# Kernel tuning notes

Hardware: AMD Instinct MI355X
Metric: run time of the kernel (lower is better)

Reference implementation:

```python
import jax, jax.numpy as jnp
import numpy as np

K_NEIGHBORS = 5
EPS = 1e-12  # torch F.normalize eps


def _l2_normalize(x):
    n = jnp.linalg.norm(x, axis=-1, keepdims=True)
    return x / jnp.maximum(n, EPS)


def setup_inputs() -> dict:
    key = jax.random.key(0)
    k1, k2, k3, k4 = jax.random.split(key, 4)
    B, D = 256, 512
    N, A = 50000, 8
    return {
        "z_flowed": jax.random.normal(k1, (B, D), dtype=jnp.float32),
        "target_attrs": jax.random.randint(k2, (B, A), 0, 3, dtype=jnp.int32),
        "train_embeddings": jax.random.normal(k3, (N, D), dtype=jnp.float32),
        "train_attributes": jax.random.randint(k4, (N, A), 0, 3, dtype=jnp.int32),
    }


def reference(z_flowed, target_attrs, train_embeddings, train_attributes):
    B = z_flowed.shape[0]
    A = target_attrs.shape[1]
    z_norm = _l2_normalize(z_flowed)          # [B, D]
    train_norm = _l2_normalize(train_embeddings)  # [N, D]

    # batched attribute match: [B, N] count of matching attributes
    match_score = (train_attributes[None, :, :] == target_attrs[:, None, :]).sum(-1)
    mask = (match_score >= (A - 1)).astype(z_norm.dtype)  # [B, N]

    # cosine similarities for all samples in one GEMM: [B, N]
    sims = jnp.einsum('nd,bd->bn', train_norm, z_norm)
    masked_sim = sims * mask

    top_k_values, _ = jax.lax.top_k(masked_sim, K_NEIGHBORS)  # [B, K]
    per_sample_loss = (1.0 - top_k_values).mean(-1)           # [B]

    # samples with fewer than k matching neighbors are skipped in the sum
    valid = (mask.sum(-1) >= K_NEIGHBORS).astype(per_sample_loss.dtype)
    return (per_sample_loss * valid).sum() / B
```

## Files before the change

kernel.cpp:

```cpp
#include <hip/hip_runtime.h>
#include <math.h>


constexpr int D = 512;
constexpr int A = 8;
constexpr int K_NEI = 5;
constexpr int CAPB = 16;
constexpr int CAP_BLK = 256;
constexpr int LDS_PAIR_CAP = 512;
constexpr int DOT_BLOCKS = 2048;

__device__ __forceinline__ float wave_reduce_add(float v) {
    #pragma unroll
    for (int m = 1; m < 64; m <<= 1) v += __shfl_xor(v, m, 64);
    return v;
}

__global__ __launch_bounds__(256) void prep_match_kernel(
    const float* __restrict__ z, const int* __restrict__ tattr,
    const int* __restrict__ trattr,
    float* __restrict__ z_norm, unsigned* __restrict__ pairs,
    int* __restrict__ cntblk, int* __restrict__ h,
    float* __restrict__ sims, float* __restrict__ out,
    int N, int NBLK, int SIMS_TOT)
{
    const int tid = threadIdx.x;

    if (blockIdx.x >= NBLK) {
        const int b = blockIdx.x - NBLK;
        if (tid < 64) {
            const int lane = tid;
            const float4* zrow = (const float4*)(z + (size_t)b * D);
            float4 v0 = zrow[lane * 2 + 0];
            float4 v1 = zrow[lane * 2 + 1];
            float ss = v0.x*v0.x + v0.y*v0.y + v0.z*v0.z + v0.w*v0.w
                     + v1.x*v1.x + v1.y*v1.y + v1.z*v1.z + v1.w*v1.w;
            ss = wave_reduce_add(ss);
            const float scale = 1.0f / fmaxf(sqrtf(ss), 1e-12f);
            v0.x *= scale; v0.y *= scale; v0.z *= scale; v0.w *= scale;
            v1.x *= scale; v1.y *= scale; v1.z *= scale; v1.w *= scale;
            float4* orow = (float4*)(z_norm + (size_t)b * D);
            orow[lane * 2 + 0] = v0;
            orow[lane * 2 + 1] = v1;
        }
        if (b == 0 && tid == 64) out[0] = 0.0f;
        float4* s4 = (float4*)sims;
        const int n4 = SIMS_TOT >> 2;
        const float4 sent = make_float4(-1e30f, -1e30f, -1e30f, -1e30f);
        for (int i = b * 256 + tid; i < n4; i += 256 * 256) s4[i] = sent;
        return;
    }

    __shared__ unsigned s_tp[256];
    __shared__ unsigned s_pairs[LDS_PAIR_CAP];
    __shared__ int s_hist[256];
    __shared__ int s_cnt;

    const int n = blockIdx.x * 256 + tid;

    {
        const int4* t4 = (const int4*)(tattr + (size_t)tid * A);
        const int4 x = t4[0], y = t4[1];
        s_tp[tid] = ((unsigned)x.x & 0xFu)        | (((unsigned)x.y & 0xFu) << 4)
                  | (((unsigned)x.z & 0xFu) << 8)  | (((unsigned)x.w & 0xFu) << 12)
                  | (((unsigned)y.x & 0xFu) << 16) | (((unsigned)y.y & 0xFu) << 20)
                  | (((unsigned)y.z & 0xFu) << 24) | (((unsigned)y.w & 0xFu) << 28);
    }
    s_hist[tid] = 0;
    if (tid == 0) s_cnt = 0;
    __syncthreads();

    if (n < N) {
        const int4* a4 = (const int4*)(trattr + (size_t)n * A);
        const int4 x = a4[0], y = a4[1];
        const unsigned p =
             ((unsigned)x.x & 0xFu)        | (((unsigned)x.y & 0xFu) << 4)
           | (((unsigned)x.z & 0xFu) << 8)  | (((unsigned)x.w & 0xFu) << 12)
           | (((unsigned)y.x & 0xFu) << 16) | (((unsigned)y.y & 0xFu) << 20)
           | (((unsigned)y.z & 0xFu) << 24) | (((unsigned)y.w & 0xFu) << 28);

        const uint4* tp4 = (const uint4*)s_tp;
        #pragma unroll 4
        for (int bq = 0; bq < 64; bq++) {
            const uint4 t = tp4[bq];
            #pragma unroll
            for (int j = 0; j < 4; j++) {
                const unsigned tv = (j == 0) ? t.x : (j == 1) ? t.y : (j == 2) ? t.z : t.w;
                const unsigned yv = p ^ tv;
                const unsigned nzhi = ((((yv & 0x77777777u) + 0x77777777u) | yv) & 0x88888888u);
                if (__popc(nzhi) <= 1) {
                    const int b = bq * 4 + j;
                    const int rank = atomicAdd(&s_hist[b], 1);
                    if (rank < CAPB) {
                        const int idx = atomicAdd(&s_cnt, 1);
                        if (idx < LDS_PAIR_CAP)
                            s_pairs[idx] = ((unsigned)n << 16)
                                         | ((unsigned)rank << 8) | (unsigned)b;
                    }
                }
            }
        }
    }
    __syncthreads();

    h[blockIdx.x * 256 + tid] = s_hist[tid];
    const int cnt = min(s_cnt, min(LDS_PAIR_CAP, CAP_BLK));
    if (tid == 0) cntblk[blockIdx.x] = cnt;
    for (int i = tid; i < cnt; i += 256)
        pairs[blockIdx.x * CAP_BLK + i] = s_pairs[i];
}

__global__ __launch_bounds__(256) void dot_kernel(
    const float* __restrict__ train, const float* __restrict__ z_norm,
    const unsigned* __restrict__ pairs, const int* __restrict__ cntblk,
    float* __restrict__ sims, int TOT, int BSTRIDE)
{
    const int tid = threadIdx.x;
    const int lane = tid & 63;
    const int q  = lane >> 4;
    const int ql = lane & 15;
    const int Q = (blockIdx.x * 4 + (tid >> 6)) * 4 + q;
    const int QTOT = DOT_BLOCKS * 16;

    for (int slot = Q; slot < TOT; slot += QTOT) {
        const int blk = slot >> 8;
        const int idx = slot & (CAP_BLK - 1);
        const bool active = (idx < cntblk[blk]);
        unsigned pr = 0;
        float ss = 0.0f, dd = 0.0f;
        if (active) {
            pr = pairs[slot];
            const int n = (int)(pr >> 16);
            const int b = (int)(pr & 255u);
            const float4* r4 = (const float4*)(train  + (size_t)n * D);
            const float4* z4 = (const float4*)(z_norm + (size_t)b * D);
            #pragma unroll
            for (int j = 0; j < 8; j++) {
                const float4 r  = r4[j * 16 + ql];
                const float4 zz = z4[j * 16 + ql];
                ss += r.x*r.x  + r.y*r.y  + r.z*r.z  + r.w*r.w;
                dd += r.x*zz.x + r.y*zz.y + r.z*zz.z + r.w*zz.w;
            }
        }
        #pragma unroll
        for (int m = 1; m < 16; m <<= 1) {
            ss += __shfl_xor(ss, m, 64);
            dd += __shfl_xor(dd, m, 64);
        }
        if (active && ql == 0) {
            const int b    = (int)(pr & 255u);
            const int rank = (int)((pr >> 8) & 255u);
            sims[(size_t)b * BSTRIDE + blk * CAPB + rank] =
                dd / fmaxf(sqrtf(ss), 1e-12f);
        }
    }
}

__global__ __launch_bounds__(64) void topk_kernel(
    const int* __restrict__ h, const float* __restrict__ sims,
    float* __restrict__ out, int NBLK, int BSTRIDE, int Bt)
{
    const int b = blockIdx.x;
    const int lane = threadIdx.x;

    int c = 0;
    for (int blk = lane; blk < NBLK; blk += 64) c += h[blk * 256 + b];
    c = (int)wave_reduce_add((float)c);

    float top[K_NEI];
    #pragma unroll
    for (int k = 0; k < K_NEI; k++) top[k] = -1e30f;
    const float* buf = sims + (size_t)b * BSTRIDE;
    for (int i = lane; i < BSTRIDE; i += 64) {
        const float v = buf[i];
        if (v > top[K_NEI - 1]) {
            top[K_NEI - 1] = v;
            #pragma unroll
            for (int k = K_NEI - 1; k > 0; k--)
                if (top[k] > top[k - 1]) { float t = top[k]; top[k] = top[k - 1]; top[k - 1] = t; }
        }
    }

    float s = 0.0f;
    #pragma unroll
    for (int r = 0; r < K_NEI; r++) {
        float M = top[0];
        #pragma unroll
        for (int m = 1; m < 64; m <<= 1) M = fmaxf(M, __shfl_xor(M, m, 64));
        s += fmaxf(M, 0.0f);
        const unsigned long long bal = __ballot(top[0] == M);
        const int first = __ffsll(bal) - 1;
        if (lane == first) {
            #pragma unroll
            for (int k = 0; k < K_NEI - 1; k++) top[k] = top[k + 1];
            top[K_NEI - 1] = -1e30f;
        }
    }

    if (lane == 0) {
        const float contrib = (c >= K_NEI) ? (1.0f - s * (1.0f / K_NEI)) : 0.0f;
        atomicAdd(out, contrib / (float)Bt);
    }
}

extern "C" void kernel_launch(void* const* d_in, const int* in_sizes, int n_in,
                              void* d_out, int out_size, void* d_ws, size_t ws_size,
                              hipStream_t stream)
{
    const float* z      = (const float*)d_in[0];
    const int*   tattr  = (const int*)d_in[1];
    const float* train  = (const float*)d_in[2];
    const int*   trattr = (const int*)d_in[3];
    float* out = (float*)d_out;

    const int B = in_sizes[0] / D;
    const int N = in_sizes[2] / D;
    const int NBLK = (N + 255) / 256;
    const int TOT = NBLK * CAP_BLK;
    const int BSTRIDE = NBLK * CAPB;
    const int SIMS_TOT = B * BSTRIDE;

    char* ws = (char*)d_ws;
    float*    z_norm  = (float*)ws;    ws += (size_t)B * D * sizeof(float);
    int*      h       = (int*)ws;      ws += (size_t)NBLK * 256 * sizeof(int);
    int*      cntblk  = (int*)ws;      ws += ((size_t)NBLK * sizeof(int) + 63) & ~63ull;
    unsigned* pairs   = (unsigned*)ws; ws += (size_t)TOT * sizeof(unsigned);
    float*    sims    = (float*)ws;

    prep_match_kernel<<<NBLK + B, 256, 0, stream>>>(
        z, tattr, trattr, z_norm, pairs, cntblk, h, sims, out, N, NBLK, SIMS_TOT);
    dot_kernel<<<DOT_BLOCKS, 256, 0, stream>>>(
        train, z_norm, pairs, cntblk, sims, TOT, BSTRIDE);
    topk_kernel<<<B, 64, 0, stream>>>(h, sims, out, NBLK, BSTRIDE, B);
}
```

Baseline: 195.7 us.

## Fuse match, dot and top-k stages into one cooperative persistent kernel

Merges the three launches into a single cooperative kernel with grid-wide syncs between the match/prep, dot-product and top-k phases, removing two kernel launch gaps. The dot phase now gives each full wave one pair instead of a quarter-wave, and applies a precomputed inverse z norm rather than storing a normalized z copy. Costs are two grid barriers and a fixed grid of 1024 blocks that must all be co-resident; the grid is assumed larger than NBLK+256 for the sentinel-fill blocks.

```diff
diff --git a/kernel.cpp b/kernel.cpp
--- a/kernel.cpp
+++ b/kernel.cpp
@@ -1,5 +1,8 @@
 #include <hip/hip_runtime.h>
+#include <hip/hip_cooperative_groups.h>
 #include <math.h>
+
+namespace cg = cooperative_groups;
 
 
 constexpr int D = 512;
@@ -8,7 +11,8 @@
 constexpr int CAPB = 16;
 constexpr int CAP_BLK = 256;
 constexpr int LDS_PAIR_CAP = 512;
-constexpr int DOT_BLOCKS = 2048;
+constexpr int GRID = 1024;
+constexpr int TPB = 256;
 
 __device__ __forceinline__ float wave_reduce_add(float v) {
     #pragma unroll
@@ -16,190 +20,180 @@
     return v;
 }
 
-__global__ __launch_bounds__(256) void prep_match_kernel(
+__global__ void __launch_bounds__(TPB, 4) mega_kernel(
     const float* __restrict__ z, const int* __restrict__ tattr,
-    const int* __restrict__ trattr,
-    float* __restrict__ z_norm, unsigned* __restrict__ pairs,
+    const float* __restrict__ train, const int* __restrict__ trattr,
+    float* __restrict__ zinv, unsigned* __restrict__ pairs,
     int* __restrict__ cntblk, int* __restrict__ h,
     float* __restrict__ sims, float* __restrict__ out,
-    int N, int NBLK, int SIMS_TOT)
+    int N, int NBLK, int Bt)
 {
+    cg::grid_group grid = cg::this_grid();
+    const int bid = blockIdx.x;
     const int tid = threadIdx.x;
-
-    if (blockIdx.x >= NBLK) {
-        const int b = blockIdx.x - NBLK;
-        if (tid < 64) {
-            const int lane = tid;
-            const float4* zrow = (const float4*)(z + (size_t)b * D);
-            float4 v0 = zrow[lane * 2 + 0];
-            float4 v1 = zrow[lane * 2 + 1];
-            float ss = v0.x*v0.x + v0.y*v0.y + v0.z*v0.z + v0.w*v0.w
-                     + v1.x*v1.x + v1.y*v1.y + v1.z*v1.z + v1.w*v1.w;
-            ss = wave_reduce_add(ss);
-            const float scale = 1.0f / fmaxf(sqrtf(ss), 1e-12f);
-            v0.x *= scale; v0.y *= scale; v0.z *= scale; v0.w *= scale;
-            v1.x *= scale; v1.y *= scale; v1.z *= scale; v1.w *= scale;
-            float4* orow = (float4*)(z_norm + (size_t)b * D);
-            orow[lane * 2 + 0] = v0;
-            orow[lane * 2 + 1] = v1;
-        }
-        if (b == 0 && tid == 64) out[0] = 0.0f;
-        float4* s4 = (float4*)sims;
-        const int n4 = SIMS_TOT >> 2;
-        const float4 sent = make_float4(-1e30f, -1e30f, -1e30f, -1e30f);
-        for (int i = b * 256 + tid; i < n4; i += 256 * 256) s4[i] = sent;
-        return;
-    }
+    const int lane = tid & 63;
+    const int wv = tid >> 6;
+    const int BSTRIDE = NBLK * CAPB;
+    const int SIMS_TOT = Bt * BSTRIDE;
 
     __shared__ unsigned s_tp[256];
     __shared__ unsigned s_pairs[LDS_PAIR_CAP];
     __shared__ int s_hist[256];
     __shared__ int s_cnt;
 
-    const int n = blockIdx.x * 256 + tid;
-
-    {
-        const int4* t4 = (const int4*)(tattr + (size_t)tid * A);
-        const int4 x = t4[0], y = t4[1];
-        s_tp[tid] = ((unsigned)x.x & 0xFu)        | (((unsigned)x.y & 0xFu) << 4)
-                  | (((unsigned)x.z & 0xFu) << 8)  | (((unsigned)x.w & 0xFu) << 12)
-                  | (((unsigned)y.x & 0xFu) << 16) | (((unsigned)y.y & 0xFu) << 20)
-                  | (((unsigned)y.z & 0xFu) << 24) | (((unsigned)y.w & 0xFu) << 28);
-    }
-    s_hist[tid] = 0;
-    if (tid == 0) s_cnt = 0;
-    __syncthreads();
-
-    if (n < N) {
-        const int4* a4 = (const int4*)(trattr + (size_t)n * A);
-        const int4 x = a4[0], y = a4[1];
-        const unsigned p =
-             ((unsigned)x.x & 0xFu)        | (((unsigned)x.y & 0xFu) << 4)
-           | (((unsigned)x.z & 0xFu) << 8)  | (((unsigned)x.w & 0xFu) << 12)
-           | (((unsigned)y.x & 0xFu) << 16) | (((unsigned)y.y & 0xFu) << 20)
-           | (((unsigned)y.z & 0xFu) << 24) | (((unsigned)y.w & 0xFu) << 28);
-
-        const uint4* tp4 = (const uint4*)s_tp;
-        #pragma unroll 4
-        for (int bq = 0; bq < 64; bq++) {
-            const uint4 t = tp4[bq];
-            #pragma unroll
-            for (int j = 0; j < 4; j++) {
-                const unsigned tv = (j == 0) ? t.x : (j == 1) ? t.y : (j == 2) ? t.z : t.w;
-                const unsigned yv = p ^ tv;
-                const unsigned nzhi = ((((yv & 0x77777777u) + 0x77777777u) | yv) & 0x88888888u);
-                if (__popc(nzhi) <= 1) {
-                    const int b = bq * 4 + j;
-                    const int rank = atomicAdd(&s_hist[b], 1);
-                    if (rank < CAPB) {
-                        const int idx = atomicAdd(&s_cnt, 1);
-                        if (idx < LDS_PAIR_CAP)
-                            s_pairs[idx] = ((unsigned)n << 16)
-                                         | ((unsigned)rank << 8) | (unsigned)b;
+    if (bid < NBLK) {
+        const int n = bid * 256 + tid;
+        {
+            const int4* t4 = (const int4*)(tattr + (size_t)tid * A);
+            const int4 x = t4[0], y = t4[1];
+            s_tp[tid] = ((unsigned)x.x & 0xFu)        | (((unsigned)x.y & 0xFu) << 4)
+                      | (((unsigned)x.z & 0xFu) << 8)  | (((unsigned)x.w & 0xFu) << 12)
+                      | (((unsigned)y.x & 0xFu) << 16) | (((unsigned)y.y & 0xFu) << 20)
+                      | (((unsigned)y.z & 0xFu) << 24) | (((unsigned)y.w & 0xFu) << 28);
+        }
+        s_hist[tid] = 0;
+        if (tid == 0) s_cnt = 0;
+        __syncthreads();
+
+        if (n < N) {
+            const int4* a4 = (const int4*)(trattr + (size_t)n * A);
+            const int4 x = a4[0], y = a4[1];
+            const unsigned p =
+                 ((unsigned)x.x & 0xFu)        | (((unsigned)x.y & 0xFu) << 4)
+               | (((unsigned)x.z & 0xFu) << 8)  | (((unsigned)x.w & 0xFu) << 12)
+               | (((unsigned)y.x & 0xFu) << 16) | (((unsigned)y.y & 0xFu) << 20)
+               | (((unsigned)y.z & 0xFu) << 24) | (((unsigned)y.w & 0xFu) << 28);
+
+            const uint4* tp4 = (const uint4*)s_tp;
+            #pragma unroll 4
+            for (int bq = 0; bq < 64; bq++) {
+                const uint4 t = tp4[bq];
+                #pragma unroll
+                for (int j = 0; j < 4; j++) {
+                    const unsigned tv = (j == 0) ? t.x : (j == 1) ? t.y
+                                      : (j == 2) ? t.z : t.w;
+                    const unsigned yv = p ^ tv;
+                    const unsigned nzhi =
+                        ((((yv & 0x77777777u) + 0x77777777u) | yv) & 0x88888888u);
+                    if (__popc(nzhi) <= 1) {
+                        const int b = bq * 4 + j;
+                        const int rank = atomicAdd(&s_hist[b], 1);
+                        if (rank < CAPB) {
+                            const int idx = atomicAdd(&s_cnt, 1);
+                            if (idx < LDS_PAIR_CAP)
+                                s_pairs[idx] = ((unsigned)n << 16)
+                                             | ((unsigned)rank << 8) | (unsigned)b;
+                        }
                     }
                 }
             }
         }
+        __syncthreads();
+        h[bid * 256 + tid] = s_hist[tid];
+        const int cnt = min(s_cnt, min(LDS_PAIR_CAP, CAP_BLK));
+        if (tid == 0) cntblk[bid] = cnt;
+        for (int i = tid; i < cnt; i += 256)
+            pairs[bid * CAP_BLK + i] = s_pairs[i];
+    } else if (bid < NBLK + 256) {
+        if (tid < 64) {
+            const int b = bid - NBLK;
+            const float4* zrow = (const float4*)(z + (size_t)b * D);
+            const float4 v0 = zrow[tid * 2 + 0];
+            const float4 v1 = zrow[tid * 2 + 1];
+            float ss = v0.x*v0.x + v0.y*v0.y + v0.z*v0.z + v0.w*v0.w
+                     + v1.x*v1.x + v1.y*v1.y + v1.z*v1.z + v1.w*v1.w;
+            ss = wave_reduce_add(ss);
+            if (tid == 0) zinv[b] = 1.0f / fmaxf(sqrtf(ss), 1e-12f);
+        }
+    } else {
+        if (bid == NBLK + 256 && tid == 0) out[0] = 0.0f;
+        float4* s4 = (float4*)sims;
+        const int n4 = SIMS_TOT >> 2;
+        const int nblocks = GRID - (NBLK + 256);
+        const float4 sent = make_float4(-1e30f, -1e30f, -1e30f, -1e30f);
+        for (int i = (bid - NBLK - 256) * TPB + tid; i < n4; i += nblocks * TPB)
+            s4[i] = sent;
     }
-    __syncthreads();
-
-    h[blockIdx.x * 256 + tid] = s_hist[tid];
-    const int cnt = min(s_cnt, min(LDS_PAIR_CAP, CAP_BLK));
-    if (tid == 0) cntblk[blockIdx.x] = cnt;
-    for (int i = tid; i < cnt; i += 256)
-        pairs[blockIdx.x * CAP_BLK + i] = s_pairs[i];
-}
-
-__global__ __launch_bounds__(256) void dot_kernel(
-    const float* __restrict__ train, const float* __restrict__ z_norm,
-    const unsigned* __restrict__ pairs, const int* __restrict__ cntblk,
-    float* __restrict__ sims, int TOT, int BSTRIDE)
-{
-    const int tid = threadIdx.x;
-    const int lane = tid & 63;
-    const int q  = lane >> 4;
-    const int ql = lane & 15;
-    const int Q = (blockIdx.x * 4 + (tid >> 6)) * 4 + q;
-    const int QTOT = DOT_BLOCKS * 16;
-
-    for (int slot = Q; slot < TOT; slot += QTOT) {
-        const int blk = slot >> 8;
-        const int idx = slot & (CAP_BLK - 1);
-        const bool active = (idx < cntblk[blk]);
-        unsigned pr = 0;
-        float ss = 0.0f, dd = 0.0f;
-        if (active) {
-            pr = pairs[slot];
-            const int n = (int)(pr >> 16);
-            const int b = (int)(pr & 255u);
-            const float4* r4 = (const float4*)(train  + (size_t)n * D);
-            const float4* z4 = (const float4*)(z_norm + (size_t)b * D);
-            #pragma unroll
-            for (int j = 0; j < 8; j++) {
-                const float4 r  = r4[j * 16 + ql];
-                const float4 zz = z4[j * 16 + ql];
-                ss += r.x*r.x  + r.y*r.y  + r.z*r.z  + r.w*r.w;
-                dd += r.x*zz.x + r.y*zz.y + r.z*zz.z + r.w*zz.w;
-            }
-        }
-        #pragma unroll
-        for (int m = 1; m < 16; m <<= 1) {
-            ss += __shfl_xor(ss, m, 64);
-            dd += __shfl_xor(dd, m, 64);
-        }
-        if (active && ql == 0) {
+
+    grid.sync();
+
+    {
+        const int w = bid * 4 + wv;
+        const int TOT = NBLK * CAP_BLK;
+        for (int slot = w; slot < TOT; slot += GRID * 4) {
+            const int blk = slot >> 8;
+            const int idx = slot & (CAP_BLK - 1);
+            if (idx >= cntblk[blk]) continue;
+            const unsigned pr = pairs[slot];
+            const int n    = (int)(pr >> 16);
             const int b    = (int)(pr & 255u);
             const int rank = (int)((pr >> 8) & 255u);
-            sims[(size_t)b * BSTRIDE + blk * CAPB + rank] =
-                dd / fmaxf(sqrtf(ss), 1e-12f);
+            const float4* r4 = (const float4*)(train + (size_t)n * D);
+            const float4* z4 = (const float4*)(z     + (size_t)b * D);
+            const float4 r0 = r4[lane * 2 + 0];
+            const float4 r1 = r4[lane * 2 + 1];
+            const float4 z0 = z4[lane * 2 + 0];
+            const float4 z1 = z4[lane * 2 + 1];
+            float ss = r0.x*r0.x + r0.y*r0.y + r0.z*r0.z + r0.w*r0.w
+                     + r1.x*r1.x + r1.y*r1.y + r1.z*r1.z + r1.w*r1.w;
+            float dd = r0.x*z0.x + r0.y*z0.y + r0.z*z0.z + r0.w*z0.w
+                     + r1.x*z1.x + r1.y*z1.y + r1.z*z1.z + r1.w*z1.w;
+            #pragma unroll
+            for (int m = 1; m < 64; m <<= 1) {
+                ss += __shfl_xor(ss, m, 64);
+                dd += __shfl_xor(dd, m, 64);
+            }
+            if (lane == 0)
+                sims[(size_t)b * BSTRIDE + blk * CAPB + rank] =
+                    dd * (1.0f / fmaxf(sqrtf(ss), 1e-12f)) * zinv[b];
         }
     }
-}
-
-__global__ __launch_bounds__(64) void topk_kernel(
-    const int* __restrict__ h, const float* __restrict__ sims,
-    float* __restrict__ out, int NBLK, int BSTRIDE, int Bt)
-{
-    const int b = blockIdx.x;
-    const int lane = threadIdx.x;
-
-    int c = 0;
-    for (int blk = lane; blk < NBLK; blk += 64) c += h[blk * 256 + b];
-    c = (int)wave_reduce_add((float)c);
-
-    float top[K_NEI];
-    #pragma unroll
-    for (int k = 0; k < K_NEI; k++) top[k] = -1e30f;
-    const float* buf = sims + (size_t)b * BSTRIDE;
-    for (int i = lane; i < BSTRIDE; i += 64) {
-        const float v = buf[i];
-        if (v > top[K_NEI - 1]) {
-            top[K_NEI - 1] = v;
+
+    grid.sync();
+
+    if (bid < Bt && tid < 64) {
+        const int b = bid;
+        int c = 0;
+        for (int blk = lane; blk < NBLK; blk += 64) c += h[blk * 256 + b];
+        #pragma unroll
+        for (int m = 1; m < 64; m <<= 1) c += __shfl_xor(c, m, 64);
+
+        float top[K_NEI];
+        #pragma unroll
+        for (int k = 0; k < K_NEI; k++) top[k] = -1e30f;
+        const float* buf = sims + (size_t)b * BSTRIDE;
+        for (int i = lane; i < BSTRIDE; i += 64) {
+            const float v = buf[i];
+            if (v > top[K_NEI - 1]) {
+                top[K_NEI - 1] = v;
+                #pragma unroll
+                for (int k = K_NEI - 1; k > 0; k--)
+                    if (top[k] > top[k - 1]) {
+                        float t = top[k]; top[k] = top[k - 1]; top[k - 1] = t;
+                    }
+            }
+        }
+
+        float s = 0.0f;
+        #pragma unroll
+        for (int r = 0; r < K_NEI; r++) {
+            float M = top[0];
             #pragma unroll
-            for (int k = K_NEI - 1; k > 0; k--)
-                if (top[k] > top[k - 1]) { float t = top[k]; top[k] = top[k - 1]; top[k - 1] = t; }
-        }
-    }
-
-    float s = 0.0f;
-    #pragma unroll
-    for (int r = 0; r < K_NEI; r++) {
-        float M = top[0];
-        #pragma unroll
-        for (int m = 1; m < 64; m <<= 1) M = fmaxf(M, __shfl_xor(M, m, 64));
-        s += fmaxf(M, 0.0f);
-        const unsigned long long bal = __ballot(top[0] == M);
-        const int first = __ffsll(bal) - 1;
-        if (lane == first) {
-            #pragma unroll
-            for (int k = 0; k < K_NEI - 1; k++) top[k] = top[k + 1];
-            top[K_NEI - 1] = -1e30f;
-        }
-    }
-
-    if (lane == 0) {
-        const float contrib = (c >= K_NEI) ? (1.0f - s * (1.0f / K_NEI)) : 0.0f;
-        atomicAdd(out, contrib / (float)Bt);
+            for (int m = 1; m < 64; m <<= 1) M = fmaxf(M, __shfl_xor(M, m, 64));
+            s += fmaxf(M, 0.0f);
+            const unsigned long long bal = __ballot(top[0] == M);
+            const int first = __ffsll(bal) - 1;
+            if (lane == first) {
+                #pragma unroll
+                for (int k = 0; k < K_NEI - 1; k++) top[k] = top[k + 1];
+                top[K_NEI - 1] = -1e30f;
+            }
+        }
+
+        if (lane == 0) {
+            const float contrib = (c >= K_NEI) ? (1.0f - s * (1.0f / K_NEI)) : 0.0f;
+            atomicAdd(out, contrib / (float)Bt);
+        }
     }
 }
 
@@ -217,19 +211,19 @@
     const int N = in_sizes[2] / D;
     const int NBLK = (N + 255) / 256;
     const int TOT = NBLK * CAP_BLK;
-    const int BSTRIDE = NBLK * CAPB;
-    const int SIMS_TOT = B * BSTRIDE;
 
     char* ws = (char*)d_ws;
-    float*    z_norm  = (float*)ws;    ws += (size_t)B * D * sizeof(float);
+    float*    zinv    = (float*)ws;    ws += ((size_t)B * sizeof(float) + 63) & ~63ull;
     int*      h       = (int*)ws;      ws += (size_t)NBLK * 256 * sizeof(int);
     int*      cntblk  = (int*)ws;      ws += ((size_t)NBLK * sizeof(int) + 63) & ~63ull;
     unsigned* pairs   = (unsigned*)ws; ws += (size_t)TOT * sizeof(unsigned);
     float*    sims    = (float*)ws;
 
-    prep_match_kernel<<<NBLK + B, 256, 0, stream>>>(
-        z, tattr, trattr, z_norm, pairs, cntblk, h, sims, out, N, NBLK, SIMS_TOT);
-    dot_kernel<<<DOT_BLOCKS, 256, 0, stream>>>(
-        train, z_norm, pairs, cntblk, sims, TOT, BSTRIDE);
-    topk_kernel<<<B, 64, 0, stream>>>(h, sims, out, NBLK, BSTRIDE, B);
+    int n_arg = N, nblk_arg = NBLK, b_arg = B;
+    void* args[] = { (void*)&z, (void*)&tattr, (void*)&train, (void*)&trattr,
+                     (void*)&zinv, (void*)&pairs, (void*)&cntblk, (void*)&h,
+                     (void*)&sims, (void*)&out,
+                     (void*)&n_arg, (void*)&nblk_arg, (void*)&b_arg };
+    hipLaunchCooperativeKernel((void*)mega_kernel, dim3(GRID), dim3(TPB),
+                               args, 0, stream);
 }
```

After: 439.7 us. 125% more time.
